# Performance work log

Measured on AMD Instinct MI355X. Metric: run time of the kernel, lower is better.

Reference implementation:

```python
import jax, jax.numpy as jnp
import numpy as np

B, NQ, NK, DM, H, DK = 8, 1024, 1024, 512, 8, 64


def setup_inputs() -> dict:
    key = jax.random.key(0)
    ks = jax.random.split(key, 20)
    s = 1.0 / np.sqrt(DM)
    inp = {
        "queries": jax.random.normal(ks[0], (B, NQ, DM), jnp.float32),
        "keys": jax.random.normal(ks[1], (B, NK, DM), jnp.float32),
        "values": jax.random.normal(ks[2], (B, NK, DM), jnp.float32),
        "attention_mask": jax.random.randint(ks[3], (B, H, NQ, NK), 0, 2).astype(bool),
        "attention_weights": jax.random.uniform(ks[4], (B, H, NQ, NK), jnp.float32),
        "memory": jax.random.uniform(ks[5], (B, NK), jnp.float32),
        "geometry": jax.random.uniform(ks[6], (B, H, NQ, NK), jnp.float32),
        "Wq": jax.random.normal(ks[7], (DM, H * DK), jnp.float32) * s,
        "bq": jnp.zeros((H * DK,), jnp.float32),
        "Wk": jax.random.normal(ks[8], (DM, H * DK), jnp.float32) * s,
        "bk": jnp.zeros((H * DK,), jnp.float32),
        "Wv": jax.random.normal(ks[9], (DM, H * DK), jnp.float32) * s,
        "bv": jnp.zeros((H * DK,), jnp.float32),
        "Wmm": jax.random.normal(ks[10], (1, H * DK), jnp.float32),
        "bmm": jnp.zeros((H * DK,), jnp.float32),
        "Wo": jax.random.normal(ks[11], (H * DK, DM), jnp.float32) * s,
        "bo": jnp.zeros((DM,), jnp.float32),
    }
    return inp


def reference(queries, keys, values, attention_mask, attention_weights, memory,
              geometry, Wq, bq, Wk, bk, Wv, bv, Wmm, bmm, Wo, bo):
    b, nq = queries.shape[:2]
    nk = keys.shape[1]
    # projections -> (b, h, n, d)
    q = (queries @ Wq + bq).reshape(b, nq, H, DK).transpose(0, 2, 1, 3)
    k = (keys @ Wk + bk).reshape(b, nk, H, DK).transpose(0, 2, 1, 3)
    v = (values @ Wv + bv).reshape(b, nk, H, DK).transpose(0, 2, 1, 3)
    # memory gate: (b, nk, 1) @ (1, h*dk) -> (b, h, nk, dk)
    mm = (memory[..., None] @ Wmm + bmm).reshape(b, nk, H, DK).transpose(0, 2, 1, 3)
    # gated scores (b, h, nq, nk)
    att = jnp.einsum('bhqd,bhkd->bhqk', q, k * mm) / np.sqrt(DK)
    att = att * attention_weights
    att = jnp.where(attention_mask, -jnp.inf, att)
    # geometric log-bias + softmax
    w_mn = jax.nn.softmax(jnp.log(jnp.clip(geometry, 1e-6)) + att, axis=-1)
    out = jnp.einsum('bhqk,bhkd->bhqd', w_mn, v * mm)
    out = out.transpose(0, 2, 1, 3).reshape(b, nq, H * DK)
    return out @ Wo + bo
```

## Files before the change

### kernel.cpp

```cpp
#include <hip/hip_runtime.h>
#include <hip/hip_bf16.h>
#include <math.h>

#define B_ 8
#define NQ_ 1024
#define NK_ 1024
#define H_ 8
#define DK_ 64
#define HDK_ 512
#define LOG2E 1.4426950408889634f

typedef _Float16 half8 __attribute__((ext_vector_type(8)));
typedef _Float16 half4 __attribute__((ext_vector_type(4)));
typedef float f32x4 __attribute__((ext_vector_type(4)));

__global__ __launch_bounds__(256)
void wtrans_kernel(const float* __restrict__ w0, const float* __restrict__ w1,
                   const float* __restrict__ w2, const float* __restrict__ w3,
                   _Float16* __restrict__ t0, _Float16* __restrict__ t1,
                   _Float16* __restrict__ t2, _Float16* __restrict__ t3,
                   const unsigned int* __restrict__ maskw, int nwords,
                   int* __restrict__ flag) {
  __shared__ float tile[64][65];
  if (blockIdx.x == 64) {
    if (blockIdx.y != 0) return;
    __shared__ int s;
    if (threadIdx.x == 0) s = 0;
    __syncthreads();
    int bad = 0;
    for (int i = threadIdx.x; i < nwords; i += blockDim.x) {
      unsigned int v = maskw[i];
      if (v > 1u && v != 0x3F800000u) bad = 1;
    }
    if (bad) atomicOr(&s, 1);
    __syncthreads();
    if (threadIdx.x == 0) *flag = s;
    return;
  }
  const float* W;
  _Float16* T;
  switch (blockIdx.y) {
    case 0: W = w0; T = t0; break;
    case 1: W = w1; T = t1; break;
    case 2: W = w2; T = t2; break;
    default: W = w3; T = t3; break;
  }
  const int t = blockIdx.x;
  const int k0 = (t >> 3) * 64, n0 = (t & 7) * 64;
  const int tid = threadIdx.x;
  const int r = tid >> 4, c4 = (tid & 15) * 4;
#pragma unroll
  for (int i = 0; i < 4; ++i) {
    const int kk = r + i * 16;
    float4 v = *(const float4*)(W + (size_t)(k0 + kk) * 512 + n0 + c4);
    tile[kk][c4 + 0] = v.x;
    tile[kk][c4 + 1] = v.y;
    tile[kk][c4 + 2] = v.z;
    tile[kk][c4 + 3] = v.w;
  }
  __syncthreads();
#pragma unroll
  for (int i = 0; i < 4; ++i) {
    const int nn = r + i * 16;
    half4 h;
#pragma unroll
    for (int j = 0; j < 4; ++j) h[j] = (_Float16)tile[c4 + j][nn];
    *(half4*)(T + (size_t)(n0 + nn) * 512 + k0 + c4) = h;
  }
}

__global__ __launch_bounds__(256)
void gemm_kernel(const float* __restrict__ A0, const float* __restrict__ A1,
                 const float* __restrict__ A2, const _Float16* __restrict__ A16,
                 const _Float16* __restrict__ B0, const _Float16* __restrict__ B1,
                 const _Float16* __restrict__ B2, const float* __restrict__ bias0,
                 const float* __restrict__ bias1, const float* __restrict__ bias2,
                 const float* __restrict__ mem, const float* __restrict__ Wmm,
                 const float* __restrict__ bmm, void* __restrict__ out0,
                 void* __restrict__ out1, void* __restrict__ out2,
                 const int mode_base) {
  __shared__ _Float16 As[128 * 32];
  __shared__ _Float16 Bs[128 * 32];
  const int mode = mode_base + blockIdx.z;
  const float* A32 = (mode == 1) ? A1 : (mode == 2) ? A2 : A0;
  const _Float16* Bt = (mode == 1) ? B1 : (mode == 2) ? B2 : B0;
  const float* bias = (mode == 1) ? bias1 : (mode == 2) ? bias2 : bias0;
  void* outp = (mode == 1) ? out1 : (mode == 2) ? out2 : out0;

  const int tid = threadIdx.x;
  const int lane = tid & 63, wave = tid >> 6;
  const int wr = wave >> 1, wc = wave & 1;
  const int l15 = lane & 15, l4 = lane >> 4;
  const int row0 = blockIdx.x * 128, col0 = blockIdx.y * 128;
  const int srow = tid >> 1;
  const int sc0 = (tid & 1) * 2;

  f32x4 acc[4][4] = {};

  for (int k0 = 0; k0 < 512; k0 += 32) {
    __syncthreads();
    const _Float16* sb = Bt + (size_t)(col0 + srow) * 512 + k0;
#pragma unroll
    for (int c = 0; c < 2; ++c) {
      int ci = sc0 + c;
      half8 ha;
      if (mode == 3) {
        ha = *(const half8*)(A16 + (size_t)(row0 + srow) * 512 + k0 + ci * 8);
      } else {
        const float* s = A32 + (size_t)(row0 + srow) * 512 + k0 + ci * 8;
        float4 x = *(const float4*)s;
        float4 y = *(const float4*)(s + 4);
        ha[0] = (_Float16)x.x; ha[1] = (_Float16)x.y;
        ha[2] = (_Float16)x.z; ha[3] = (_Float16)x.w;
        ha[4] = (_Float16)y.x; ha[5] = (_Float16)y.y;
        ha[6] = (_Float16)y.z; ha[7] = (_Float16)y.w;
      }
      float4 vb = *(const float4*)(sb + ci * 8);
      int cd = ci ^ (srow & 3);
      *(half8*)((char*)As + srow * 64 + (cd << 4)) = ha;
      *(float4*)((char*)Bs + srow * 64 + (cd << 4)) = vb;
    }
    __syncthreads();
    half8 af[4], bf[4];
#pragma unroll
    for (int mi = 0; mi < 4; ++mi) {
      int r = wr * 64 + mi * 16 + l15;
      af[mi] = *(half8*)((char*)As + r * 64 + ((l4 ^ (r & 3)) << 4));
    }
#pragma unroll
    for (int ni = 0; ni < 4; ++ni) {
      int r = wc * 64 + ni * 16 + l15;
      bf[ni] = *(half8*)((char*)Bs + r * 64 + ((l4 ^ (r & 3)) << 4));
    }
#pragma unroll
    for (int mi = 0; mi < 4; ++mi)
#pragma unroll
      for (int ni = 0; ni < 4; ++ni)
        acc[mi][ni] =
            __builtin_amdgcn_mfma_f32_16x16x32_f16(af[mi], bf[ni], acc[mi][ni], 0, 0, 0);
  }

#pragma unroll
  for (int mi = 0; mi < 4; ++mi) {
#pragma unroll
    for (int ni = 0; ni < 4; ++ni) {
      const int gc = col0 + wc * 64 + ni * 16 + l15;
      const float bi = bias[gc];
      const int h = gc >> 6, d = gc & 63;
#pragma unroll
      for (int reg = 0; reg < 4; ++reg) {
        const int gr = row0 + wr * 64 + mi * 16 + l4 * 4 + reg;
        float val = acc[mi][ni][reg] + bi;
        if (mode == 3) {
          ((float*)outp)[(size_t)gr * 512 + gc] = val;
        } else if (mode == 0) {
          const int b = gr >> 10, n = gr & 1023;
          ((_Float16*)outp)[((size_t)(b * 8 + h) * 1024 + n) * 64 + d] =
              (_Float16)(val * (LOG2E / 8.0f));
        } else {
          const int b = gr >> 10, n = gr & 1023;
          float mmv = fmaf(mem[gr], Wmm[gc], bmm[gc]);
          float g = val * mmv;
          if (mode == 1)
            ((_Float16*)outp)[((size_t)(b * 8 + h) * 1024 + n) * 64 + d] = (_Float16)g;
          else
            ((_Float16*)outp)[((size_t)(b * 8 + h) * 64 + d) * 1024 + n] = (_Float16)g;
        }
      }
    }
  }
}

__global__ __launch_bounds__(256, 2)
void attn_kernel(const _Float16* __restrict__ Qp, const _Float16* __restrict__ Kg,
                 const _Float16* __restrict__ Vgt, const float* __restrict__ attw,
                 const float* __restrict__ geom, const void* __restrict__ maskp,
                 const int* __restrict__ flagp, _Float16* __restrict__ Ocat) {
  __shared__ _Float16 Kbuf[2][64 * 64];
  __shared__ _Float16 Vbuf[2][64 * 64];
  __shared__ _Float16 Ps[4][16 * 64];

  const int tid = threadIdx.x;
  const int lane = tid & 63, wave = tid >> 6;
  const int l15 = lane & 15, l4 = lane >> 4;
  const int bid = blockIdx.x;
  const int qt = bid >> 6;
  const int g = bid & 63;
  const int h = g & 7, b = g >> 3;
  const int bh = b * H_ + h;
  const int qb = qt * 64 + wave * 16;
  const int kq = qb + l15;
  const int maskBytes = *flagp;
  const unsigned char* m8 = (const unsigned char*)maskp;
  const int* m32 = (const int*)maskp;

  half8 aq[2];
  {
    const _Float16* qsrc = Qp + ((size_t)bh * NQ_ + kq) * DK_;
#pragma unroll
    for (int s = 0; s < 2; ++s) aq[s] = *(const half8*)(qsrc + s * 32 + l4 * 8);
  }

  f32x4 fo[4] = {};
  float mrun = -INFINITY, lrun = 0.f;

  const size_t wgBase = ((size_t)bh << 20) + (size_t)kq * NK_ + l4 * 4;

  const int srL = lane >> 3;
  const int sci = lane & 7;
  auto stageKV = [&](int kt, int sel) {
    const char* kgb = (const char*)(Kg + ((size_t)bh * NK_ + kt * 64) * DK_);
    const char* vgb = (const char*)(Vgt + (size_t)bh * DK_ * NK_ + kt * 64);
#pragma unroll
    for (int i = 0; i < 2; ++i) {
      const int rbase = wave * 16 + i * 8;
      const int r = rbase + srL;
      const char* src = kgb + (size_t)r * 128 + ((sci ^ (r & 7)) << 4);
      __builtin_amdgcn_global_load_lds(src, (char*)&Kbuf[sel][0] + rbase * 128, 16, 0, 0);
    }
#pragma unroll
    for (int i = 0; i < 2; ++i) {
      const int rbase = wave * 16 + i * 8;
      const int r = rbase + srL;
      const char* src = vgb + (size_t)r * (NK_ * 2) + ((sci ^ (r & 7)) << 4);
      __builtin_amdgcn_global_load_lds(src, (char*)&Vbuf[sel][0] + rbase * 128, 16, 0, 0);
    }
  };

  float4 wv[4], gv[4];
  unsigned mk;
  auto loadWG = [&](int kt) {
    const size_t base = wgBase + (size_t)kt * 64;
    unsigned m = 0;
#pragma unroll
    for (int c = 0; c < 4; ++c) {
      wv[c] = *(const float4*)(attw + base + c * 16);
      gv[c] = *(const float4*)(geom + base + c * 16);
      if (maskBytes) {
        unsigned v = *(const unsigned*)(m8 + base + c * 16);
        m |= (((v & 0xffu) ? 1u : 0u) | ((v & 0xff00u) ? 2u : 0u) |
              ((v & 0xff0000u) ? 4u : 0u) | ((v & 0xff000000u) ? 8u : 0u)) << (c * 4);
      } else {
        int4 v = *(const int4*)(m32 + base + c * 16);
        m |= ((v.x ? 1u : 0u) | (v.y ? 2u : 0u) | (v.z ? 4u : 0u) | (v.w ? 8u : 0u))
             << (c * 4);
      }
    }
    mk = m;
  };

  stageKV(0, 0);
  loadWG(0);
  __syncthreads();

#pragma unroll 2
  for (int kt = 0; kt < 16; ++kt) {
    const int sel = kt & 1;
    if (kt + 1 < 16) stageKV(kt + 1, sel ^ 1);

    const char* Kb = (const char*)&Kbuf[sel][0];
    const char* Vb = (const char*)&Vbuf[sel][0];

    f32x4 sf[4];
    __builtin_amdgcn_s_setprio(1);
#pragma unroll
    for (int c = 0; c < 4; ++c) {
      sf[c] = (f32x4){0.f, 0.f, 0.f, 0.f};
#pragma unroll
      for (int s = 0; s < 2; ++s) {
        int r = c * 16 + l15;
        half8 ak = *(half8*)(Kb + r * 128 + (((s * 4 + l4) ^ (r & 7)) << 4));
        sf[c] = __builtin_amdgcn_mfma_f32_16x16x32_f16(ak, aq[s], sf[c], 0, 0, 0);
      }
    }
    __builtin_amdgcn_s_setprio(0);

    float mx = -INFINITY;
#pragma unroll
    for (int c = 0; c < 4; ++c)
#pragma unroll
      for (int reg = 0; reg < 4; ++reg) {
        float sv = sf[c][reg] * wv[c][reg];
        sf[c][reg] = sv;
        mx = fmaxf(mx, sv);
      }
    mx = fmaxf(mx, __shfl_xor(mx, 16));
    mx = fmaxf(mx, __shfl_xor(mx, 32));
    const float mn = fmaxf(mrun, mx);
    const float sc = (mrun == -INFINITY) ? 0.f : exp2f(mrun - mn);
    mrun = mn;

    float rs = 0.f;
#pragma unroll
    for (int c = 0; c < 4; ++c)
#pragma unroll
      for (int reg = 0; reg < 4; ++reg) {
        float p = fmaxf(gv[c][reg], 1e-6f) * exp2f(sf[c][reg] - mn);
        p = ((mk >> (c * 4 + reg)) & 1u) ? 0.f : p;
        sf[c][reg] = p;
        rs += p;
      }

    if (kt + 1 < 16) loadWG(kt + 1);

#pragma unroll
    for (int c = 0; c < 4; ++c)
#pragma unroll
      for (int reg = 0; reg < 4; ++reg) fo[c][reg] *= sc;
    lrun = lrun * sc + rs;

    char* pw = (char*)&Ps[wave][0];
#pragma unroll
    for (int c = 0; c < 4; ++c) {
      half4 hp;
#pragma unroll
      for (int reg = 0; reg < 4; ++reg) hp[reg] = (_Float16)sf[c][reg];
      int ci = c * 2 + (l4 >> 1);
      *(half4*)(pw + l15 * 128 + ((ci ^ (l15 & 7)) << 4) + (l4 & 1) * 8) = hp;
    }

    __builtin_amdgcn_s_setprio(1);
#pragma unroll
    for (int s4 = 0; s4 < 2; ++s4) {
      half8 pa = *(half8*)(pw + l15 * 128 + (((s4 * 4 + l4) ^ (l15 & 7)) << 4));
#pragma unroll
      for (int c = 0; c < 4; ++c) {
        int rd = c * 16 + l15;
        half8 bv = *(half8*)(Vb + rd * 128 + (((s4 * 4 + l4) ^ (rd & 7)) << 4));
        fo[c] = __builtin_amdgcn_mfma_f32_16x16x32_f16(bv, pa, fo[c], 0, 0, 0);
      }
    }
    __builtin_amdgcn_s_setprio(0);

    __syncthreads();
  }

  float lsum = lrun;
  lsum += __shfl_xor(lsum, 16);
  lsum += __shfl_xor(lsum, 32);
  const float rinv = 1.0f / lsum;

  _Float16* orow = Ocat + ((size_t)b * NQ_ + kq) * HDK_ + h * DK_;
#pragma unroll
  for (int c = 0; c < 4; ++c) {
    half4 hv;
#pragma unroll
    for (int reg = 0; reg < 4; ++reg) hv[reg] = (_Float16)(fo[c][reg] * rinv);
    *(half4*)(orow + c * 16 + l4 * 4) = hv;
  }
}

extern "C" void kernel_launch(void* const* d_in, const int* in_sizes, int n_in,
                              void* d_out, int out_size, void* d_ws, size_t ws_size,
                              hipStream_t stream) {
  (void)in_sizes; (void)n_in; (void)out_size; (void)ws_size;
  const float* queries = (const float*)d_in[0];
  const float* keys    = (const float*)d_in[1];
  const float* values  = (const float*)d_in[2];
  const void*  maskp   = d_in[3];
  const float* attw    = (const float*)d_in[4];
  const float* memo    = (const float*)d_in[5];
  const float* geom    = (const float*)d_in[6];
  const float* Wq = (const float*)d_in[7];
  const float* bq = (const float*)d_in[8];
  const float* Wk = (const float*)d_in[9];
  const float* bk = (const float*)d_in[10];
  const float* Wv = (const float*)d_in[11];
  const float* bv = (const float*)d_in[12];
  const float* Wmm = (const float*)d_in[13];
  const float* bmm = (const float*)d_in[14];
  const float* Wo = (const float*)d_in[15];
  const float* bo = (const float*)d_in[16];

  char* ws = (char*)d_ws;
  size_t off = 0;
  auto alloc = [&](size_t bytes) {
    char* p = ws + off;
    off += (bytes + 255) & ~(size_t)255;
    return p;
  };
  const size_t MAT = (size_t)8192 * 512 * 2;
  int* flag = (int*)alloc(256);
  _Float16* Wtq = (_Float16*)alloc((size_t)512 * 512 * 2);
  _Float16* Wtk = (_Float16*)alloc((size_t)512 * 512 * 2);
  _Float16* Wtv = (_Float16*)alloc((size_t)512 * 512 * 2);
  _Float16* Wto = (_Float16*)alloc((size_t)512 * 512 * 2);
  _Float16* Qp   = (_Float16*)alloc(MAT);
  _Float16* Kgp  = (_Float16*)alloc(MAT);
  _Float16* Vgtp = (_Float16*)alloc(MAT);
  _Float16* Ocat = (_Float16*)alloc(MAT);

  wtrans_kernel<<<dim3(65, 4), 256, 0, stream>>>(Wq, Wk, Wv, Wo, Wtq, Wtk, Wtv, Wto,
                                                 (const unsigned int*)maskp, 4096, flag);

  gemm_kernel<<<dim3(64, 4, 3), 256, 0, stream>>>(
      queries, keys, values, nullptr, Wtq, Wtk, Wtv, bq, bk, bv, memo, Wmm, bmm,
      Qp, Kgp, Vgtp, 0);

  attn_kernel<<<1024, 256, 0, stream>>>(Qp, Kgp, Vgtp, attw, geom, maskp, flag, Ocat);

  gemm_kernel<<<dim3(64, 4, 1), 256, 0, stream>>>(
      nullptr, nullptr, nullptr, Ocat, Wto, nullptr, nullptr, bo, nullptr, nullptr,
      nullptr, nullptr, nullptr, d_out, nullptr, nullptr, 3);
}
```

Measured before the change: 319.9 us.

## Load K/V tiles directly into registers instead of LDS double-buffering

Removes the shared-memory staging of K and V tiles, and the block-wide barrier that went with it. Each wave now loads its K and V MFMA operands straight from global memory into registers, prefetching the next tile after the current MFMAs finish. Launch bounds go up to 3 blocks per CU because LDS use drops. The cost is that each of the four waves now fetches the full K/V tile separately, so global/L2 traffic for K/V is four times higher, and register pressure rises under the tighter occupancy bound.

```diff
diff --git a/kernel.cpp b/kernel.cpp
--- a/kernel.cpp
+++ b/kernel.cpp
@@ -171,13 +171,11 @@
   }
 }
 
-__global__ __launch_bounds__(256, 2)
+__global__ __launch_bounds__(256, 3)
 void attn_kernel(const _Float16* __restrict__ Qp, const _Float16* __restrict__ Kg,
                  const _Float16* __restrict__ Vgt, const float* __restrict__ attw,
                  const float* __restrict__ geom, const void* __restrict__ maskp,
                  const int* __restrict__ flagp, _Float16* __restrict__ Ocat) {
-  __shared__ _Float16 Kbuf[2][64 * 64];
-  __shared__ _Float16 Vbuf[2][64 * 64];
   __shared__ _Float16 Ps[4][16 * 64];
 
   const int tid = threadIdx.x;
@@ -204,27 +202,28 @@
   f32x4 fo[4] = {};
   float mrun = -INFINITY, lrun = 0.f;
 
+  const _Float16* Kbase = Kg + (size_t)bh * NK_ * DK_;
+  const _Float16* Vbase = Vgt + (size_t)bh * DK_ * NK_;
   const size_t wgBase = ((size_t)bh << 20) + (size_t)kq * NK_ + l4 * 4;
 
-  const int srL = lane >> 3;
-  const int sci = lane & 7;
-  auto stageKV = [&](int kt, int sel) {
-    const char* kgb = (const char*)(Kg + ((size_t)bh * NK_ + kt * 64) * DK_);
-    const char* vgb = (const char*)(Vgt + (size_t)bh * DK_ * NK_ + kt * 64);
-#pragma unroll
-    for (int i = 0; i < 2; ++i) {
-      const int rbase = wave * 16 + i * 8;
-      const int r = rbase + srL;
-      const char* src = kgb + (size_t)r * 128 + ((sci ^ (r & 7)) << 4);
-      __builtin_amdgcn_global_load_lds(src, (char*)&Kbuf[sel][0] + rbase * 128, 16, 0, 0);
-    }
-#pragma unroll
-    for (int i = 0; i < 2; ++i) {
-      const int rbase = wave * 16 + i * 8;
-      const int r = rbase + srL;
-      const char* src = vgb + (size_t)r * (NK_ * 2) + ((sci ^ (r & 7)) << 4);
-      __builtin_amdgcn_global_load_lds(src, (char*)&Vbuf[sel][0] + rbase * 128, 16, 0, 0);
-    }
+  half8 ak[2][4];
+  auto loadK = [&](int kt) {
+    const _Float16* kp = Kbase + (size_t)(kt * 64 + l15) * DK_ + l4 * 8;
+#pragma unroll
+    for (int c = 0; c < 4; ++c)
+#pragma unroll
+      for (int s = 0; s < 2; ++s)
+        ak[s][c] = *(const half8*)(kp + (size_t)(c * 16) * DK_ + s * 32);
+  };
+
+  half8 av[2][4];
+  auto loadV = [&](int kt) {
+    const _Float16* vp = Vbase + (size_t)l15 * NK_ + kt * 64 + l4 * 8;
+#pragma unroll
+    for (int s4 = 0; s4 < 2; ++s4)
+#pragma unroll
+      for (int c = 0; c < 4; ++c)
+        av[s4][c] = *(const half8*)(vp + (size_t)(c * 16) * NK_ + s4 * 32);
   };
 
   float4 wv[4], gv[4];
@@ -249,31 +248,23 @@
     mk = m;
   };
 
-  stageKV(0, 0);
+  loadK(0);
+  loadV(0);
   loadWG(0);
-  __syncthreads();
-
-#pragma unroll 2
+
   for (int kt = 0; kt < 16; ++kt) {
-    const int sel = kt & 1;
-    if (kt + 1 < 16) stageKV(kt + 1, sel ^ 1);
-
-    const char* Kb = (const char*)&Kbuf[sel][0];
-    const char* Vb = (const char*)&Vbuf[sel][0];
-
     f32x4 sf[4];
     __builtin_amdgcn_s_setprio(1);
 #pragma unroll
     for (int c = 0; c < 4; ++c) {
       sf[c] = (f32x4){0.f, 0.f, 0.f, 0.f};
 #pragma unroll
-      for (int s = 0; s < 2; ++s) {
-        int r = c * 16 + l15;
-        half8 ak = *(half8*)(Kb + r * 128 + (((s * 4 + l4) ^ (r & 7)) << 4));
-        sf[c] = __builtin_amdgcn_mfma_f32_16x16x32_f16(ak, aq[s], sf[c], 0, 0, 0);
-      }
+      for (int s = 0; s < 2; ++s)
+        sf[c] = __builtin_amdgcn_mfma_f32_16x16x32_f16(ak[s][c], aq[s], sf[c], 0, 0, 0);
     }
     __builtin_amdgcn_s_setprio(0);
+
+    if (kt + 1 < 16) loadK(kt + 1);
 
     float mx = -INFINITY;
 #pragma unroll
@@ -324,15 +315,12 @@
     for (int s4 = 0; s4 < 2; ++s4) {
       half8 pa = *(half8*)(pw + l15 * 128 + (((s4 * 4 + l4) ^ (l15 & 7)) << 4));
 #pragma unroll
-      for (int c = 0; c < 4; ++c) {
-        int rd = c * 16 + l15;
-        half8 bv = *(half8*)(Vb + rd * 128 + (((s4 * 4 + l4) ^ (rd & 7)) << 4));
-        fo[c] = __builtin_amdgcn_mfma_f32_16x16x32_f16(bv, pa, fo[c], 0, 0, 0);
-      }
+      for (int c = 0; c < 4; ++c)
+        fo[c] = __builtin_amdgcn_mfma_f32_16x16x32_f16(av[s4][c], pa, fo[c], 0, 0, 0);
     }
     __builtin_amdgcn_s_setprio(0);
 
-    __syncthreads();
+    if (kt + 1 < 16) loadV(kt + 1);
   }
 
   float lsum = lrun;
```

Result: slower. 603.7 us (+88.7%).
